# Optimization experiments

Measured on AMD Instinct MI355X. Metric: run time of the kernel, lower is better.

Reference implementation:

```python
import jax, jax.numpy as jnp
import numpy as np

N_NODES = 500_000
N_EDGES = 2_000_000
N_GRAPHS = 20_000
N_PAIRS = 50_000
IN_CH = 64
EMB_CH = 64
HID_CH = 256
OUT_CH = 1


def setup_inputs() -> dict:
    key = jax.random.key(0)
    ks = jax.random.split(key, 10)
    x = jax.random.normal(ks[0], (N_NODES, IN_CH), dtype=jnp.float32)
    edge_index = jax.random.randint(ks[1], (2, N_EDGES), 0, N_NODES, dtype=jnp.int64)
    batch_idx = jnp.sort(jax.random.randint(ks[2], (N_NODES,), 0, N_GRAPHS, dtype=jnp.int64))
    drug_pairs = jax.random.randint(ks[3], (2, N_PAIRS), 0, N_GRAPHS, dtype=jnp.int64)
    s1 = 1.0 / np.sqrt(IN_CH)
    s2 = 1.0 / np.sqrt(EMB_CH)
    s3 = 1.0 / np.sqrt(2 * EMB_CH)
    s4 = 1.0 / np.sqrt(HID_CH)
    return {
        "x": x,
        "edge_index": edge_index,
        "batch_idx": batch_idx,
        "drug_pairs": drug_pairs,
        "W1": jax.random.normal(ks[4], (IN_CH, EMB_CH), jnp.float32) * s1,
        "b1": jnp.zeros((EMB_CH,), jnp.float32),
        "W2": jax.random.normal(ks[5], (EMB_CH, EMB_CH), jnp.float32) * s2,
        "b2": jnp.zeros((EMB_CH,), jnp.float32),
        "Wr1": jax.random.normal(ks[6], (2 * EMB_CH, HID_CH), jnp.float32) * s3,
        "br1": jnp.zeros((HID_CH,), jnp.float32),
        "Wr2": jax.random.normal(ks[7], (HID_CH, OUT_CH), jnp.float32) * s4,
        "br2": jnp.zeros((OUT_CH,), jnp.float32),
    }


def _gcn_conv(x, W, b, src, dst, num_nodes):
    # Standard GCNConv: x' = D^{-1/2} (A + I) D^{-1/2} (x W) + b,
    # with D the degree including self-loops.
    h = x @ W  # [N, C_out]
    ones = jnp.ones((src.shape[0],), h.dtype)
    deg = jax.ops.segment_sum(ones, dst, num_segments=num_nodes) + 1.0  # self-loop
    inv_sqrt = jax.lax.rsqrt(deg)
    norm = inv_sqrt[src] * inv_sqrt[dst]  # [E]
    msg = h[src] * norm[:, None]  # gather + scale, [E, C_out]
    agg = jax.ops.segment_sum(msg, dst, num_segments=num_nodes)
    agg = agg + h * (1.0 / deg)[:, None]  # self-loop term (norm = deg^{-1})
    return agg + b


def reference(x, edge_index, batch_idx, drug_pairs, W1, b1, W2, b2, Wr1, br1, Wr2, br2):
    n = x.shape[0]
    src, dst = edge_index[0], edge_index[1]
    # conv1 -> relu -> dropout(eval: identity)
    h = jax.nn.relu(_gcn_conv(x, W1, b1, src, dst, n))
    # conv2 -> relu -> dropout(eval: identity)
    h = jax.nn.relu(_gcn_conv(h, W2, b2, src, dst, n))
    # scatter_mean pooling: node embeds -> per-graph mean
    sums = jax.ops.segment_sum(h, batch_idx, num_segments=N_GRAPHS)
    counts = jax.ops.segment_sum(jnp.ones((n,), h.dtype), batch_idx, num_segments=N_GRAPHS)
    graph_embeds = sums / jnp.maximum(counts, 1.0)[:, None]  # [G, C]
    # gather drug pair embeddings and concat
    pair_feat = jnp.concatenate(
        [graph_embeds[drug_pairs[0]], graph_embeds[drug_pairs[1]]], axis=-1
    )  # [P, 2C]
    hid = jax.nn.relu(pair_feat @ Wr1 + br1)
    return hid @ Wr2 + br2  # [P, out_channels]
```

## Files before the change

kernel.cpp:

```cpp
#include <hip/hip_runtime.h>
#include <cstdint>

#define N_GRAPHS 20000
#define SCAN_CHUNK 2048
#define NBLK 512
#define SRC_BITS 19

typedef _Float16 half_t;
typedef __attribute__((ext_vector_type(4))) _Float16 half4;
typedef __attribute__((ext_vector_type(8))) _Float16 half8;
typedef __attribute__((ext_vector_type(4))) float f32x4;

__global__ __launch_bounds__(256) void scan1(const int* __restrict__ in, int* __restrict__ out,
                                             int* __restrict__ bsum, int M) {
  __shared__ int lds[256];
  int t = threadIdx.x;
  int base = blockIdx.x * SCAN_CHUNK + t * 8;
  int v[8];
  int s = 0;
#pragma unroll
  for (int i = 0; i < 8; ++i) {
    v[i] = (base + i < M) ? in[base + i] : 0;
    s += v[i];
  }
  lds[t] = s;
  __syncthreads();
  for (int off = 1; off < 256; off <<= 1) {
    int x = (t >= off) ? lds[t - off] : 0;
    __syncthreads();
    lds[t] += x;
    __syncthreads();
  }
  if (t == 255) bsum[blockIdx.x] = lds[255];
  int run = (t > 0) ? lds[t - 1] : 0;
#pragma unroll
  for (int i = 0; i < 8; ++i) {
    if (base + i <= M) out[base + i] = run;
    run += v[i];
  }
}

__global__ __launch_bounds__(256) void scan2(int* __restrict__ bsum, int nb) {
  __shared__ int lds[256];
  int t = threadIdx.x;
  lds[t] = (t < nb) ? bsum[t] : 0;
  __syncthreads();
  for (int off = 1; off < 256; off <<= 1) {
    int x = (t >= off) ? lds[t - off] : 0;
    __syncthreads();
    lds[t] += x;
    __syncthreads();
  }
  if (t < nb) bsum[t] = (t > 0) ? lds[t - 1] : 0;
}

__global__ void scan3(int* __restrict__ out, const int* __restrict__ bsum, int Mp1) {
  int i = blockIdx.x * blockDim.x + threadIdx.x;
  if (i < Mp1) out[i] += bsum[i / SCAN_CHUNK];
}

__global__ __launch_bounds__(256) void bucket_hist(const int* __restrict__ dst,
                                                   int* __restrict__ bcnt, int E, int nbuck) {
  __shared__ int h[512];
  for (int i = threadIdx.x; i < 512; i += 256) h[i] = 0;
  __syncthreads();
  int per = (E + NBLK - 1) / NBLK;
  int s = blockIdx.x * per;
  int e = min(s + per, E);
  for (int i = s + threadIdx.x; i < e; i += 256) atomicAdd(&h[dst[i] >> 10], 1);
  __syncthreads();
  for (int b = threadIdx.x; b < nbuck; b += 256) bcnt[(long)b * NBLK + blockIdx.x] = h[b];
}

__global__ __launch_bounds__(256) void bucket_scatter(const int* __restrict__ src,
                                                      const int* __restrict__ dst,
                                                      const int* __restrict__ bbase,
                                                      int* __restrict__ sed, int E, int nbuck) {
  __shared__ int h[512];
  for (int b = threadIdx.x; b < nbuck; b += 256) h[b] = bbase[(long)b * NBLK + blockIdx.x];
  __syncthreads();
  int per = (E + NBLK - 1) / NBLK;
  int s = blockIdx.x * per;
  int e = min(s + per, E);
  for (int i = s + threadIdx.x; i < e; i += 256) {
    int d = dst[i];
    int pos = atomicAdd(&h[d >> 10], 1);
    sed[pos] = ((d & 1023) << SRC_BITS) | src[i];
  }
}

__global__ __launch_bounds__(256) void node_csr(const int* __restrict__ sed,
                                                const int* __restrict__ bbase,
                                                int2* __restrict__ rsp, float* __restrict__ isq,
                                                int* __restrict__ csr, int E, int nbuck, int N,
                                                int PARK) {
  __shared__ int h[1024];
  __shared__ int ws[256];
  __shared__ int cur[1024];
  int b = blockIdx.x;
  int n0 = b << 10;
  int nn = min(1024, N - n0);
  int t = threadIdx.x;
  for (int i = t; i < 1024; i += 256) h[i] = 0;
  __syncthreads();
  int s = bbase[(long)b * NBLK];
  int e = (b + 1 < nbuck) ? bbase[(long)(b + 1) * NBLK] : E;
  for (int i = s + t; i < e; i += 256) atomicAdd(&h[((unsigned)sed[i]) >> SRC_BITS], 1);
  __syncthreads();
  int v0 = h[4 * t], v1 = h[4 * t + 1], v2 = h[4 * t + 2], v3 = h[4 * t + 3];
  int p0 = (v0 + 3) & ~3, p1 = (v1 + 3) & ~3, p2 = (v2 + 3) & ~3, p3 = (v3 + 3) & ~3;
  ws[t] = p0 + p1 + p2 + p3;
  __syncthreads();
  for (int off = 1; off < 256; off <<= 1) {
    int x = (t >= off) ? ws[t - off] : 0;
    __syncthreads();
    ws[t] += x;
    __syncthreads();
  }
  int pbase = s + 3072 * b;
  int st0 = pbase + ((t > 0) ? ws[t - 1] : 0);
  int st1 = st0 + p0, st2 = st1 + p1, st3 = st2 + p2;
  int i0 = 4 * t;
  cur[i0] = st0;
  cur[i0 + 1] = st1;
  cur[i0 + 2] = st2;
  cur[i0 + 3] = st3;
  if (i0 < nn) { rsp[n0 + i0] = make_int2(st0, st0 + p0); isq[n0 + i0] = rsqrtf((float)(v0 + 1)); }
  if (i0 + 1 < nn) { rsp[n0 + i0 + 1] = make_int2(st1, st1 + p1); isq[n0 + i0 + 1] = rsqrtf((float)(v1 + 1)); }
  if (i0 + 2 < nn) { rsp[n0 + i0 + 2] = make_int2(st2, st2 + p2); isq[n0 + i0 + 2] = rsqrtf((float)(v2 + 1)); }
  if (i0 + 3 < nn) { rsp[n0 + i0 + 3] = make_int2(st3, st3 + p3); isq[n0 + i0 + 3] = rsqrtf((float)(v3 + 1)); }
  __syncthreads();
  for (int i = s + t; i < e; i += 256) {
    int v = sed[i];
    int pos = atomicAdd(&cur[((unsigned)v) >> SRC_BITS], 1);
    csr[pos] = v & ((1 << SRC_BITS) - 1);
  }
  __syncthreads();
  for (int j = v0; j < p0; ++j) csr[st0 + j] = N;
  for (int j = v1; j < p1; ++j) csr[st1 + j] = N;
  for (int j = v2; j < p2; ++j) csr[st2 + j] = N;
  for (int j = v3; j < p3; ++j) csr[st3 + j] = N;
  if (b == 0 && t < 64) csr[PARK + t] = N;
}

__global__ __launch_bounds__(256) void scale_cast(const float* __restrict__ x,
                                                  const float* __restrict__ isq,
                                                  half_t* __restrict__ xs1,
                                                  half_t* __restrict__ xs2,
                                                  long nocts, int N) {
  long i = (long)blockIdx.x * 256 + threadIdx.x;
  if (blockIdx.x == 0 && threadIdx.x < 16) {
    const half8 z = {(half_t)0, (half_t)0, (half_t)0, (half_t)0,
                     (half_t)0, (half_t)0, (half_t)0, (half_t)0};
    half_t* base = (threadIdx.x < 8) ? xs1 : xs2;
    ((half8*)(base + (size_t)N * 64))[threadIdx.x & 7] = z;
  }
  if (i >= nocts) return;
  int node = (int)(i >> 3);
  float s = isq[node];
  float4 vlo = ((const float4*)x)[i * 2];
  float4 vhi = ((const float4*)x)[i * 2 + 1];
  half8 h;
  h[0] = (half_t)(vlo.x * s);
  h[1] = (half_t)(vlo.y * s);
  h[2] = (half_t)(vlo.z * s);
  h[3] = (half_t)(vlo.w * s);
  h[4] = (half_t)(vhi.x * s);
  h[5] = (half_t)(vhi.y * s);
  h[6] = (half_t)(vhi.z * s);
  h[7] = (half_t)(vhi.w * s);
  ((half8*)xs1)[i] = h;
}

__global__ __launch_bounds__(256) void gather_fused(const half_t* __restrict__ xs,
                                                    const int* __restrict__ csr,
                                                    const int2* __restrict__ rsp,
                                                    const float* __restrict__ isq,
                                                    const float* __restrict__ W,
                                                    const float* __restrict__ bias,
                                                    half_t* __restrict__ out, int N,
                                                    int PARK, int scale_out) {
  __shared__ half_t Wt[64][72];
  __shared__ half_t exh[32][72];
  __shared__ float idv[32];
  int tid = threadIdx.x;
  {
    int c = tid & 63;
    int kb = (tid >> 6) * 16;
#pragma unroll
    for (int i = 0; i < 16; ++i) Wt[c][kb + i] = (half_t)W[(kb + i) * 64 + c];
  }

  int lane = tid & 63;
  int sub = lane & 7;
  int grp = lane >> 3;
  int li = tid >> 3;
  int wid = (blockIdx.x * blockDim.x + tid) >> 6;
  long d0 = (long)wid * 8;
  int d = (int)d0 + grp;
  bool vd = (d0 < N) && (d < N);
  int dd = vd ? d : N - 1;
  int2 rr = rsp[dd];
  int jj = vd ? rr.x : PARK;
  int je = vd ? rr.y : PARK;
  float id = isq[dd];
  const uint8_t* xb = (const uint8_t*)xs;
  uint32_t co = (uint32_t)sub << 4;
  float ac[8];
  {
    half8 sv = *(const half8*)(xb + (((uint32_t)dd << 7) + co));
#pragma unroll
    for (int c = 0; c < 8; ++c) ac[c] = (float)sv[c];
  }
  jj = (jj < je) ? jj : PARK;
  while (__any(jj != PARK)) {
    int s0 = csr[jj];
    int s1 = csr[jj + 1];
    int s2 = csr[jj + 2];
    int s3 = csr[jj + 3];
    half8 v0 = *(const half8*)(xb + (((uint32_t)s0 << 7) + co));
    half8 v1 = *(const half8*)(xb + (((uint32_t)s1 << 7) + co));
    half8 v2 = *(const half8*)(xb + (((uint32_t)s2 << 7) + co));
    half8 v3 = *(const half8*)(xb + (((uint32_t)s3 << 7) + co));
    half8 sum = (v0 + v1) + (v2 + v3);
#pragma unroll
    for (int c = 0; c < 8; ++c) ac[c] += (float)sum[c];
    jj += 4;
    jj = (jj < je) ? jj : PARK;
  }
  {
    half8 ah;
#pragma unroll
    for (int c = 0; c < 8; ++c) ah[c] = (half_t)ac[c];
    *(half8*)&exh[li][sub * 8] = ah;
    if (sub == 0) idv[li] = id;
  }
  __syncthreads();

  int w = tid >> 6;
  int lr = lane & 15;
  int lk = lane >> 4;
  long d0b = (long)blockIdx.x * 32;
#pragma unroll
  for (int t2 = 0; t2 < 2; ++t2) {
    int tile = w * 2 + t2;
    int mt = tile >> 2;
    int nt = tile & 3;
    f32x4 acc = {0.f, 0.f, 0.f, 0.f};
#pragma unroll
    for (int ks = 0; ks < 2; ++ks) {
      half8 a = *(const half8*)&exh[mt * 16 + lr][ks * 32 + lk * 8];
      half8 b = *(const half8*)&Wt[nt * 16 + lr][ks * 32 + lk * 8];
      acc = __builtin_amdgcn_mfma_f32_16x16x32_f16(a, b, acc, 0, 0, 0);
    }
    float bv = bias[nt * 16 + lr];
#pragma unroll
    for (int j = 0; j < 4; ++j) {
      int nl = mt * 16 + lk * 4 + j;
      long dn = d0b + nl;
      if (dn < N) {
        float id2 = idv[nl];
        float m = scale_out ? id2 : 1.f;
        float r = fmaxf(fmaf(acc[j], id2, bv), 0.f) * m;
        out[dn * 64 + nt * 16 + lr] = (half_t)r;
      }
    }
  }
}

__global__ void seg_offsets(const int* __restrict__ batch, int* __restrict__ off, int N, int G) {
  int i = blockIdx.x * blockDim.x + threadIdx.x;
  if (i >= N) return;
  int b = batch[i];
  if (i == 0) {
    for (int g = 0; g <= b; ++g) off[g] = 0;
  } else {
    int pb = batch[i - 1];
    for (int g = pb + 1; g <= b; ++g) off[g] = i;
  }
  if (i == N - 1) {
    for (int g = b + 1; g <= G; ++g) off[g] = N;
  }
}

__global__ void pool_mean(const half_t* __restrict__ e2, const int* __restrict__ off,
                          float* __restrict__ ge, int G) {
  int lane = threadIdx.x & 63;
  int wid = (blockIdx.x * blockDim.x + threadIdx.x) >> 6;
  int nw = (gridDim.x * blockDim.x) >> 6;
  int c8 = lane & 7;
  int rp = lane >> 3;
  for (int g = wid; g < G; g += nw) {
    int s = off[g];
    int e = off[g + 1];
    float acc[8];
#pragma unroll
    for (int c = 0; c < 8; ++c) acc[c] = 0.f;
    for (int n = s + rp; n < e; n += 8) {
      half8 v = *(const half8*)&e2[(long)n * 64 + c8 * 8];
#pragma unroll
      for (int c = 0; c < 8; ++c) acc[c] += (float)v[c];
    }
#pragma unroll
    for (int c = 0; c < 8; ++c) {
      acc[c] += __shfl_xor(acc[c], 8, 64);
      acc[c] += __shfl_xor(acc[c], 16, 64);
      acc[c] += __shfl_xor(acc[c], 32, 64);
    }
    if (rp == 0) {
      float inv = 1.f / fmaxf((float)(e - s), 1.f);
      float4 lo = make_float4(acc[0] * inv, acc[1] * inv, acc[2] * inv, acc[3] * inv);
      float4 hi = make_float4(acc[4] * inv, acc[5] * inv, acc[6] * inv, acc[7] * inv);
      *(float4*)&ge[(long)g * 64 + c8 * 8] = lo;
      *(float4*)&ge[(long)g * 64 + c8 * 8 + 4] = hi;
    }
  }
}

#define PPB 256
__global__ __launch_bounds__(256) void pair_mlp(const float* __restrict__ ge,
                                                const int* __restrict__ dp,
                                                const float* __restrict__ Wr1,
                                                const float* __restrict__ br1,
                                                const float* __restrict__ Wr2,
                                                const float* __restrict__ br2,
                                                float* __restrict__ out, int P) {
  __shared__ half_t Wt[256][136];
  __shared__ half_t ft[PPB][136];
  int tid = threadIdx.x;
  for (int idx = tid; idx < 128 * 256; idx += 256) {
    int k = idx >> 8;
    int j = idx & 255;
    Wt[j][k] = (half_t)Wr1[idx];
  }
  int base = blockIdx.x * PPB;
  {
    int pp = base + tid;
    bool v = pp < P;
    int ga = v ? dp[pp] : 0;
    int gb = v ? dp[P + pp] : 0;
#pragma unroll
    for (int h = 0; h < 8; ++h) {
      const float* srow = (h < 4) ? &ge[(long)ga * 64 + h * 16] : &ge[(long)gb * 64 + (h - 4) * 16];
      float4 a0 = *(const float4*)&srow[0];
      float4 a1 = *(const float4*)&srow[4];
      float4 a2 = *(const float4*)&srow[8];
      float4 a3 = *(const float4*)&srow[12];
      half8 h0, h1;
      h0[0] = (half_t)a0.x; h0[1] = (half_t)a0.y; h0[2] = (half_t)a0.z; h0[3] = (half_t)a0.w;
      h0[4] = (half_t)a1.x; h0[5] = (half_t)a1.y; h0[6] = (half_t)a1.z; h0[7] = (half_t)a1.w;
      h1[0] = (half_t)a2.x; h1[1] = (half_t)a2.y; h1[2] = (half_t)a2.z; h1[3] = (half_t)a2.w;
      h1[4] = (half_t)a3.x; h1[5] = (half_t)a3.y; h1[6] = (half_t)a3.z; h1[7] = (half_t)a3.w;
      *(half8*)&ft[tid][h * 16] = h0;
      *(half8*)&ft[tid][h * 16 + 8] = h1;
    }
  }
  __syncthreads();

  int w = tid >> 6;
  int lane = tid & 63;
  int lr = lane & 15;
  int lk = lane >> 4;
  float b1v[16], w2v[16];
#pragma unroll
  for (int nt = 0; nt < 16; ++nt) {
    b1v[nt] = br1[nt * 16 + lr];
    w2v[nt] = Wr2[nt * 16 + lr];
  }
  float br2v = br2[0];
#pragma unroll
  for (int m4 = 0; m4 < 4; ++m4) {
    int mt = w * 4 + m4;
    float ps0 = 0.f, ps1 = 0.f, ps2 = 0.f, ps3 = 0.f;
#pragma unroll
    for (int nt = 0; nt < 16; ++nt) {
      f32x4 acc = {0.f, 0.f, 0.f, 0.f};
#pragma unroll
      for (int ks = 0; ks < 4; ++ks) {
        half8 a = *(const half8*)&ft[mt * 16 + lr][ks * 32 + lk * 8];
        half8 b = *(const half8*)&Wt[nt * 16 + lr][ks * 32 + lk * 8];
        acc = __builtin_amdgcn_mfma_f32_16x16x32_f16(a, b, acc, 0, 0, 0);
      }
      ps0 += fmaxf(acc[0] + b1v[nt], 0.f) * w2v[nt];
      ps1 += fmaxf(acc[1] + b1v[nt], 0.f) * w2v[nt];
      ps2 += fmaxf(acc[2] + b1v[nt], 0.f) * w2v[nt];
      ps3 += fmaxf(acc[3] + b1v[nt], 0.f) * w2v[nt];
    }
#pragma unroll
    for (int o = 1; o < 16; o <<= 1) {
      ps0 += __shfl_xor(ps0, o, 64);
      ps1 += __shfl_xor(ps1, o, 64);
      ps2 += __shfl_xor(ps2, o, 64);
      ps3 += __shfl_xor(ps3, o, 64);
    }
    if (lr == 0) {
      int prow = mt * 16 + lk * 4;
      int pp = base + prow;
      if (pp + 0 < P) out[pp + 0] = ps0 + br2v;
      if (pp + 1 < P) out[pp + 1] = ps1 + br2v;
      if (pp + 2 < P) out[pp + 2] = ps2 + br2v;
      if (pp + 3 < P) out[pp + 3] = ps3 + br2v;
    }
  }
}

extern "C" void kernel_launch(void* const* d_in, const int* in_sizes, int n_in,
                              void* d_out, int out_size, void* d_ws, size_t ws_size,
                              hipStream_t stream) {
  const float* x = (const float*)d_in[0];
  const int* ei = (const int*)d_in[1];
  const int* batch = (const int*)d_in[2];
  const int* dp = (const int*)d_in[3];
  const float* W1 = (const float*)d_in[4];
  const float* b1 = (const float*)d_in[5];
  const float* W2 = (const float*)d_in[6];
  const float* b2 = (const float*)d_in[7];
  const float* Wr1 = (const float*)d_in[8];
  const float* br1 = (const float*)d_in[9];
  const float* Wr2 = (const float*)d_in[10];
  const float* br2 = (const float*)d_in[11];
  float* out = (float*)d_out;

  int N = in_sizes[0] / 64;
  int E = in_sizes[1] / 2;
  int P = in_sizes[3] / 2;
  int G = N_GRAPHS;
  const int* src = ei;
  const int* dstp = ei + E;

  int nbuck = (N + 1023) >> 10;
  long M = (long)nbuck * NBLK;
  int PARK = E + 3072 * nbuck;

  char* ws = (char*)d_ws;
  size_t o = 0;
  auto alloc = [&](size_t bytes) {
    void* p = ws + o;
    o += (bytes + 255) & ~(size_t)255;
    return p;
  };
  float* isq = (float*)alloc((size_t)N * 4);
  int2* rsp = (int2*)alloc((size_t)N * 8);
  int* bsum = (int*)alloc(1024 * 4);
  int* goff = (int*)alloc((size_t)(G + 1) * 4);
  int* bcnt = (int*)alloc((size_t)(M + 1) * 4);
  int* sed = (int*)alloc((size_t)E * 4);
  int* csr = (int*)alloc((size_t)(PARK + 80) * 4);
  half_t* xs1 = (half_t*)alloc((size_t)(N + 1) * 64 * 2);
  half_t* xs2 = (half_t*)alloc((size_t)(N + 1) * 64 * 2);
  half_t* abuf = (half_t*)alloc((size_t)N * 64 * 2);
  float* ge = (float*)alloc((size_t)G * 64 * 4);

  bucket_hist<<<NBLK, 256, 0, stream>>>(dstp, bcnt, E, nbuck);
  int nbA = (int)((M + SCAN_CHUNK - 1) / SCAN_CHUNK);
  scan1<<<nbA, 256, 0, stream>>>(bcnt, bcnt, bsum, (int)M);
  scan2<<<1, 256, 0, stream>>>(bsum, nbA);
  scan3<<<(int)((M + 1 + 255) / 256), 256, 0, stream>>>(bcnt, bsum, (int)(M + 1));
  bucket_scatter<<<NBLK, 256, 0, stream>>>(src, dstp, bcnt, sed, E, nbuck);
  node_csr<<<nbuck, 256, 0, stream>>>(sed, bcnt, rsp, isq, csr, E, nbuck, N, PARK);
  seg_offsets<<<(N + 255) / 256, 256, 0, stream>>>(batch, goff, N, G);

  long nocts = (long)N * 8;
  int gblocks = (N + 31) / 32;
  scale_cast<<<(int)((nocts + 255) / 256), 256, 0, stream>>>(x, isq, xs1, xs2, nocts, N);
  gather_fused<<<gblocks, 256, 0, stream>>>(xs1, csr, rsp, isq, W1, b1, xs2, N, PARK, 1);
  gather_fused<<<gblocks, 256, 0, stream>>>(xs2, csr, rsp, isq, W2, b2, abuf, N, PARK, 0);
  pool_mean<<<2048, 256, 0, stream>>>(abuf, goff, ge, G);
  pair_mlp<<<(P + PPB - 1) / PPB, 256, 0, stream>>>(ge, dp, Wr1, br1, Wr2, br2, out, P);
}
```

Measured before the change: 275.3 us.

## Bin nodes by degree and process gather in degree-sorted order

```diff
diff --git a/kernel.cpp b/kernel.cpp
--- a/kernel.cpp
+++ b/kernel.cpp
@@ -141,6 +141,40 @@
   for (int j = v2; j < p2; ++j) csr[st2 + j] = N;
   for (int j = v3; j < p3; ++j) csr[st3 + j] = N;
   if (b == 0 && t < 64) csr[PARK + t] = N;
+}
+
+__global__ __launch_bounds__(256) void bin_hist(const int2* __restrict__ rsp,
+                                                int* __restrict__ bcnt2, int N) {
+  __shared__ int h[16];
+  if (threadIdx.x < 16) h[threadIdx.x] = 0;
+  __syncthreads();
+  int per = (N + NBLK - 1) / NBLK;
+  int s = blockIdx.x * per;
+  int e = min(s + per, N);
+  for (int i = s + threadIdx.x; i < e; i += 256) {
+    int2 rr = rsp[i];
+    int it = (rr.y - rr.x) >> 2;
+    atomicAdd(&h[min(it, 15)], 1);
+  }
+  __syncthreads();
+  if (threadIdx.x < 16) bcnt2[(long)threadIdx.x * NBLK + blockIdx.x] = h[threadIdx.x];
+}
+
+__global__ __launch_bounds__(256) void bin_scatter(const int2* __restrict__ rsp,
+                                                   const int* __restrict__ bbase2,
+                                                   int* __restrict__ perm, int N) {
+  __shared__ int h[16];
+  if (threadIdx.x < 16) h[threadIdx.x] = bbase2[(long)threadIdx.x * NBLK + blockIdx.x];
+  __syncthreads();
+  int per = (N + NBLK - 1) / NBLK;
+  int s = blockIdx.x * per;
+  int e = min(s + per, N);
+  for (int i = s + threadIdx.x; i < e; i += 256) {
+    int2 rr = rsp[i];
+    int it = (rr.y - rr.x) >> 2;
+    int pos = atomicAdd(&h[min(it, 15)], 1);
+    perm[pos] = i;
+  }
 }
 
 __global__ __launch_bounds__(256) void scale_cast(const float* __restrict__ x,
@@ -176,6 +210,7 @@
                                                     const int* __restrict__ csr,
                                                     const int2* __restrict__ rsp,
                                                     const float* __restrict__ isq,
+                                                    const int* __restrict__ perm,
                                                     const float* __restrict__ W,
                                                     const float* __restrict__ bias,
                                                     half_t* __restrict__ out, int N,
@@ -183,6 +218,7 @@
   __shared__ half_t Wt[64][72];
   __shared__ half_t exh[32][72];
   __shared__ float idv[32];
+  __shared__ int pnv[32];
   int tid = threadIdx.x;
   {
     int c = tid & 63;
@@ -196,10 +232,10 @@
   int grp = lane >> 3;
   int li = tid >> 3;
   int wid = (blockIdx.x * blockDim.x + tid) >> 6;
-  long d0 = (long)wid * 8;
-  int d = (int)d0 + grp;
-  bool vd = (d0 < N) && (d < N);
-  int dd = vd ? d : N - 1;
+  long i0 = (long)wid * 8;
+  long idx = i0 + grp;
+  bool vd = (i0 < N) && (idx < N);
+  int dd = vd ? perm[idx] : (N - 1);
   int2 rr = rsp[dd];
   int jj = vd ? rr.x : PARK;
   int je = vd ? rr.y : PARK;
@@ -233,14 +269,16 @@
 #pragma unroll
     for (int c = 0; c < 8; ++c) ah[c] = (half_t)ac[c];
     *(half8*)&exh[li][sub * 8] = ah;
-    if (sub == 0) idv[li] = id;
+    if (sub == 0) {
+      idv[li] = id;
+      pnv[li] = vd ? dd : -1;
+    }
   }
   __syncthreads();
 
   int w = tid >> 6;
   int lr = lane & 15;
   int lk = lane >> 4;
-  long d0b = (long)blockIdx.x * 32;
 #pragma unroll
   for (int t2 = 0; t2 < 2; ++t2) {
     int tile = w * 2 + t2;
@@ -257,12 +295,12 @@
 #pragma unroll
     for (int j = 0; j < 4; ++j) {
       int nl = mt * 16 + lk * 4 + j;
-      long dn = d0b + nl;
-      if (dn < N) {
+      int pn = pnv[nl];
+      if (pn >= 0) {
         float id2 = idv[nl];
         float m = scale_out ? id2 : 1.f;
         float r = fmaxf(fmaf(acc[j], id2, bv), 0.f) * m;
-        out[dn * 64 + nt * 16 + lr] = (half_t)r;
+        out[(long)pn * 64 + nt * 16 + lr] = (half_t)r;
       }
     }
   }
@@ -430,6 +468,7 @@
 
   int nbuck = (N + 1023) >> 10;
   long M = (long)nbuck * NBLK;
+  long M2 = 16L * NBLK;
   int PARK = E + 3072 * nbuck;
 
   char* ws = (char*)d_ws;
@@ -441,9 +480,11 @@
   };
   float* isq = (float*)alloc((size_t)N * 4);
   int2* rsp = (int2*)alloc((size_t)N * 8);
+  int* perm = (int*)alloc((size_t)N * 4);
   int* bsum = (int*)alloc(1024 * 4);
   int* goff = (int*)alloc((size_t)(G + 1) * 4);
   int* bcnt = (int*)alloc((size_t)(M + 1) * 4);
+  int* bcnt2 = (int*)alloc((size_t)(M2 + 1) * 4);
   int* sed = (int*)alloc((size_t)E * 4);
   int* csr = (int*)alloc((size_t)(PARK + 80) * 4);
   half_t* xs1 = (half_t*)alloc((size_t)(N + 1) * 64 * 2);
@@ -458,13 +499,19 @@
   scan3<<<(int)((M + 1 + 255) / 256), 256, 0, stream>>>(bcnt, bsum, (int)(M + 1));
   bucket_scatter<<<NBLK, 256, 0, stream>>>(src, dstp, bcnt, sed, E, nbuck);
   node_csr<<<nbuck, 256, 0, stream>>>(sed, bcnt, rsp, isq, csr, E, nbuck, N, PARK);
+  bin_hist<<<NBLK, 256, 0, stream>>>(rsp, bcnt2, N);
+  int nbB = (int)((M2 + SCAN_CHUNK - 1) / SCAN_CHUNK);
+  scan1<<<nbB, 256, 0, stream>>>(bcnt2, bcnt2, bsum, (int)M2);
+  scan2<<<1, 256, 0, stream>>>(bsum, nbB);
+  scan3<<<(int)((M2 + 1 + 255) / 256), 256, 0, stream>>>(bcnt2, bsum, (int)(M2 + 1));
+  bin_scatter<<<NBLK, 256, 0, stream>>>(rsp, bcnt2, perm, N);
   seg_offsets<<<(N + 255) / 256, 256, 0, stream>>>(batch, goff, N, G);
 
   long nocts = (long)N * 8;
   int gblocks = (N + 31) / 32;
   scale_cast<<<(int)((nocts + 255) / 256), 256, 0, stream>>>(x, isq, xs1, xs2, nocts, N);
-  gather_fused<<<gblocks, 256, 0, stream>>>(xs1, csr, rsp, isq, W1, b1, xs2, N, PARK, 1);
-  gather_fused<<<gblocks, 256, 0, stream>>>(xs2, csr, rsp, isq, W2, b2, abuf, N, PARK, 0);
+  gather_fused<<<gblocks, 256, 0, stream>>>(xs1, csr, rsp, isq, perm, W1, b1, xs2, N, PARK, 1);
+  gather_fused<<<gblocks, 256, 0, stream>>>(xs2, csr, rsp, isq, perm, W2, b2, abuf, N, PARK, 0);
   pool_mean<<<2048, 256, 0, stream>>>(abuf, goff, ge, G);
   pair_mlp<<<(P + PPB - 1) / PPB, 256, 0, stream>>>(ge, dp, Wr1, br1, Wr2, br2, out, P);
 }
```

New measurement: 300.9 us. 9.3% more time.
